# Kernel tuning notes

Measured on AMD Instinct MI355X. Metric: run time of the kernel, lower is better.

Reference implementation:

```python
import jax, jax.numpy as jnp
import numpy as np


def _expand_chunk(x):
    # prepend the previous bucket along the chunk axis: [b, nb, bl, ...] -> [b, nb, 2*bl, ...]
    return jnp.concatenate([jnp.roll(x, 1, axis=1), x], axis=2)


def _gather_seq(origin, idx):
    # origin [b, s, d], idx [b, s, r] -> out[b, s, :, r] = origin[b, idx[b, s, r], :]
    b = origin.shape[0]
    g = origin[jnp.arange(b)[:, None, None], idx]  # [b, s, r, d]
    return jnp.transpose(g, (0, 1, 3, 2))          # [b, s, d, r]


def _count_dup_keys(inp, rounds):
    # inp [b, s, K] int32: count duplicate key indices within a window of `rounds` in sorted order
    sort_idx = jnp.argsort(inp, axis=2)
    sorted_k = jnp.take_along_axis(inp, sort_idx, axis=2)
    unsort = jnp.argsort(sort_idx, axis=2)
    cnt = jnp.ones(inp.shape, jnp.float32)
    for i in range(1, rounds):
        eq = (sorted_k[..., i:] == sorted_k[..., :-i]).astype(jnp.float32)
        pad = jnp.zeros(inp.shape[:-1] + (i,), jnp.float32)
        cnt = cnt + jnp.concatenate([pad, eq], axis=-1) + jnp.concatenate([eq, pad], axis=-1)
    return jnp.take_along_axis(cnt, unsort, axis=2)


def setup_inputs() -> dict:
    key = jax.random.key(0)
    k1, k2, k3 = jax.random.split(key, 3)
    B_M_H, SEQ, D_K, N_ROUNDS, N_BUCKETS = 32, 2048, 64, 4, 32
    query = jax.random.normal(k1, (B_M_H, SEQ, D_K), jnp.float32)
    value = jax.random.normal(k2, (B_M_H, SEQ, D_K), jnp.float32)
    rand_matrix = jax.random.normal(k3, (B_M_H, D_K, N_ROUNDS, N_BUCKETS // 2), jnp.float32)
    return {"query": query, "value": value, "rand_matrix": rand_matrix}


def reference(query, value, rand_matrix):
    b, s, d = query.shape
    nr = rand_matrix.shape[2]
    n_buckets = 2 * rand_matrix.shape[3]
    bl = s // n_buckets  # bucket_len

    # --- LSH hashing: argmax over [proj, -proj], then make hashes unique per position ---
    proj = jnp.einsum('bsd,bdrk->bsrk', query, rand_matrix)
    hashes = jnp.argmax(jnp.concatenate([proj, -proj], axis=-1), axis=-1).astype(jnp.int32)
    hashes = hashes * s + jnp.arange(s, dtype=jnp.int32)[None, :, None]  # [b, s, nr]

    sort_idx = jnp.argsort(hashes, axis=1)      # [b, s, nr]
    unsort_idx = jnp.argsort(sort_idx, axis=1)  # [b, s, nr]

    # --- sort queries into buckets ---
    q = _gather_seq(query, sort_idx).reshape(b, n_buckets, bl, d, nr)
    k = _expand_chunk(q)  # [b, nb, 2*bl, d, nr]
    k = k * jax.lax.rsqrt(jnp.maximum(jnp.sum(k * k, axis=-2, keepdims=True), 1e-12))

    qk = jnp.einsum('bnidr,bnjdr->bnijr', q, k) / np.float32(np.sqrt(d))  # [b, nb, bl, 2bl, nr]

    # --- causal / self masks on original positions ---
    qi = sort_idx.reshape(b, n_buckets, bl, nr) % s
    ki = _expand_chunk(qi)  # [b, nb, 2bl, nr]
    mask1 = (qi[:, :, :, None, :] < ki[:, :, None, :, :]).astype(jnp.float32)
    mask2 = (qi[:, :, :, None, :] == ki[:, :, None, :, :]).astype(jnp.float32)
    qk = qk * (1 - mask1) + mask1 * (-1e9)
    qk = qk * (1 - mask2) + mask2 * (-1e5)

    # --- duplicate-key counting across rounds ---
    ki_b = jnp.broadcast_to(ki[:, :, None, :, :], (b, n_buckets, bl, 2 * bl, nr)).reshape(b, s, 2 * bl * nr)
    count_keys = _count_dup_keys(ki_b, nr).reshape(b, s, 2 * bl, nr)

    qk = qk.reshape(b, s, 2 * bl, nr)
    lse = jax.scipy.special.logsumexp(qk, axis=2)  # [b, s, nr]
    sm = jnp.exp(qk - lse[:, :, None, :]) / count_keys

    v = _gather_seq(value, sort_idx).reshape(b, n_buckets, bl, d, nr)
    vk = _expand_chunk(v)  # [b, nb, 2bl, d, nr]
    sm = sm.reshape(b, n_buckets, bl, 2 * bl, nr)
    att = jnp.einsum('bnijr,bnjdr->bnidr', sm, vk).reshape(b, s, d, nr)

    # --- unsort back to original order, per round ---
    att = jnp.transpose(att, (0, 1, 3, 2))  # [b, s, nr, d]
    att = jnp.take_along_axis(att, jnp.broadcast_to(unsort_idx[:, :, :, None], att.shape), axis=1)
    lse = jnp.take_along_axis(lse, unsort_idx, axis=1)

    # --- combine rounds weighted by softmax of logsumexp ---
    w = jax.nn.softmax(lse, axis=-1)  # [b, s, nr]
    return jnp.einsum('bsrd,bsr->bsd', att, w)
```

## Files before the change

### kernel.cpp

```cpp
#include <hip/hip_runtime.h>

typedef unsigned short u16;
typedef unsigned int   u32;
typedef short bf16x8 __attribute__((ext_vector_type(8)));
typedef float f32x16 __attribute__((ext_vector_type(16)));

#define S_  2048
#define D_  64
#define NR_ 4
#define NB_ 32

#define AS 72
#define VS 136
#define PS 136

__device__ __forceinline__ float bf2f(u16 u){ return __uint_as_float(((u32)u)<<16); }
__device__ __forceinline__ u16 f2bf(float f){
  u32 u = __float_as_uint(f);
  u32 r = (u + 0x7fffu + ((u>>16)&1u)) >> 16;
  return (u16)r;
}
__device__ __forceinline__ void unpack2(u32 w, float &a, float &b){
  a = __uint_as_float(w<<16);
  b = __uint_as_float(w & 0xffff0000u);
}
__device__ __forceinline__ bf16x8 ld8(const u16* p){
  union { uint4 u; bf16x8 v; } x;
  x.u = *(const uint4*)p;
  return x.v;
}

__global__ __launch_bounds__(256) void k_hash(const float* __restrict__ q,
                                              const float* __restrict__ R,
                                              int* __restrict__ hout){
  __shared__ float Rl[64][64];
  int b   = blockIdx.x >> 3;
  int pos = (blockIdx.x & 7) * 256 + threadIdx.x;
  const float* Rb = R + (size_t)b * 4096;
  for (int idx = threadIdx.x; idx < 4096; idx += 256)
    Rl[idx >> 6][idx & 63] = Rb[idx];
  __syncthreads();

  const float4* q4 = (const float4*)(q + ((size_t)b * S_ + pos) * D_);
  float acc[64];
  #pragma unroll
  for (int i = 0; i < 64; i++) acc[i] = 0.f;

  #pragma unroll
  for (int c = 0; c < 16; c++){
    float4 w = q4[c];
    float qd[4] = {w.x, w.y, w.z, w.w};
    #pragma unroll
    for (int dd = 0; dd < 4; dd++){
      int d = c * 4 + dd;
      const float4* Rr = (const float4*)(&Rl[d][0]);
      #pragma unroll
      for (int k4 = 0; k4 < 16; k4++){
        float4 rv = Rr[k4];
        acc[k4*4+0] += qd[dd] * rv.x;
        acc[k4*4+1] += qd[dd] * rv.y;
        acc[k4*4+2] += qd[dd] * rv.z;
        acc[k4*4+3] += qd[dd] * rv.w;
      }
    }
  }
  #pragma unroll
  for (int r = 0; r < 4; r++){
    float bv = acc[r*16]; int bi = 0;
    #pragma unroll
    for (int m = 1; m < 32; m++){
      float v = (m < 16) ? acc[r*16 + m] : -acc[r*16 + m - 16];
      if (v > bv){ bv = v; bi = m; }
    }
    hout[((size_t)b * NR_ + r) * S_ + pos] = bi;
  }
}

__global__ __launch_bounds__(256) void k_sort(const int* __restrict__ h,
                                              int* __restrict__ sidx,
                                              int* __restrict__ chk){
  __shared__ int cnt[32][257];
  __shared__ int base[32];
  int br = blockIdx.x;
  const int* hb = h + (size_t)br * S_;
  int t = threadIdx.x;

  #pragma unroll
  for (int hh = 0; hh < 32; hh++) cnt[hh][t] = 0;
  __syncthreads();

  int hv[8];
  const int4* hb4 = (const int4*)hb;
  int4 a0 = hb4[t*2], a1 = hb4[t*2+1];
  hv[0]=a0.x; hv[1]=a0.y; hv[2]=a0.z; hv[3]=a0.w;
  hv[4]=a1.x; hv[5]=a1.y; hv[6]=a1.z; hv[7]=a1.w;
  #pragma unroll
  for (int k = 0; k < 8; k++) cnt[hv[k]][t]++;
  __syncthreads();

  int wave = t >> 6, lane = t & 63;
  for (int hh = wave*8; hh < wave*8 + 8; hh++){
    int vals[4]; int s0 = 0;
    #pragma unroll
    for (int k = 0; k < 4; k++){ vals[k] = cnt[hh][lane*4+k]; s0 += vals[k]; }
    int incl = s0;
    #pragma unroll
    for (int off = 1; off < 64; off <<= 1){
      int o = __shfl_up(incl, off, 64);
      if (lane >= off) incl += o;
    }
    int run = incl - s0;
    #pragma unroll
    for (int k = 0; k < 4; k++){ int tmp = vals[k]; cnt[hh][lane*4+k] = run; run += tmp; }
    if (lane == 63) base[hh] = incl;
  }
  __syncthreads();
  if (t == 0){
    int run = 0;
    #pragma unroll
    for (int hh = 0; hh < 32; hh++){ int tot = base[hh]; base[hh] = run; run += tot; }
  }
  __syncthreads();

  int p0 = t * 8;
  #pragma unroll
  for (int k = 0; k < 8; k++){
    int hh = hv[k];
    int c = cnt[hh][t];
    int slot = base[hh] + c;
    cnt[hh][t] = c + 1;
    sidx[(size_t)br * S_ + slot]    = p0 + k;
    chk [(size_t)br * S_ + p0 + k]  = slot >> 6;
  }
}

__global__ __launch_bounds__(256, 4) void k_attn(const float* __restrict__ q,
                                                 const float* __restrict__ v,
                                                 const int* __restrict__ sidx,
                                                 const int* __restrict__ chk,
                                                 float* __restrict__ lse_ws,
                                                 u16*  __restrict__ att_ws){
  __shared__ u16 A[128*AS];
  __shared__ u16 SM[64*PS];
  __shared__ int   pkey[128];
  __shared__ float rcnt[128];
  __shared__ float sc[128];

  int blk = blockIdx.x;
  int b = blk >> 7, r = (blk >> 5) & 3, n = blk & 31;
  int npv = (n + 31) & 31;
  int t = threadIdx.x;
  int lane = t & 63, w = t >> 6;
  const int* sb = sidx + ((size_t)b * NR_ + r) * S_;

  if (t < 128){
    int p = (t < 64) ? sb[npv*64 + t] : sb[n*64 + (t - 64)];
    pkey[t] = p;
    int c = 0;
    #pragma unroll
    for (int rr = 0; rr < 4; rr++){
      int ch = chk[((size_t)b * NR_ + rr) * S_ + p];
      c += (ch == n) || (ch == npv);
    }
    if (c < 1) c = 1;
    rcnt[t] = 1.0f / (float)c;
  }
  __syncthreads();

  int row = t >> 1, half = t & 1;
  float4 qv[8];
  {
    const float4* src = (const float4*)(q + ((size_t)b*S_ + pkey[row])*D_) + half*8;
    #pragma unroll
    for (int k = 0; k < 8; k++) qv[k] = src[k];
  }
  int jp = t & 63, dgrp = t >> 6;
  float4 va[4], vb[4];
  {
    const float4* s0 = (const float4*)(v + ((size_t)b*S_ + pkey[2*jp  ])*D_) + dgrp*4;
    const float4* s1 = (const float4*)(v + ((size_t)b*S_ + pkey[2*jp+1])*D_) + dgrp*4;
    #pragma unroll
    for (int k = 0; k < 4; k++){ va[k] = s0[k]; vb[k] = s1[k]; }
  }
  {
    float ss = 0.f;
    u32 buf[16];
    #pragma unroll
    for (int k = 0; k < 8; k++){
      float4 f = qv[k];
      u16 b0 = f2bf(f.x), b1 = f2bf(f.y), b2 = f2bf(f.z), b3 = f2bf(f.w);
      float g0 = bf2f(b0), g1 = bf2f(b1), g2 = bf2f(b2), g3 = bf2f(b3);
      ss += g0*g0 + g1*g1 + g2*g2 + g3*g3;
      buf[k*2]   = (u32)b0 | ((u32)b1 << 16);
      buf[k*2+1] = (u32)b2 | ((u32)b3 << 16);
    }
    uint4* dst = (uint4*)(&A[row*AS + half*32]);
    #pragma unroll
    for (int k = 0; k < 4; k++)
      dst[k] = make_uint4(buf[4*k], buf[4*k+1], buf[4*k+2], buf[4*k+3]);
    float ss2 = ss + __shfl_xor(ss, 1, 64);
    if (half == 0) sc[row] = rsqrtf(fmaxf(ss2, 1e-12f)) * 0.125f;
  }
  __syncthreads();

  int Mt = w & 1, Nt0 = (w >> 1) * 2;
  f32x16 acc0, acc1;
  #pragma unroll
  for (int i = 0; i < 16; i++){ acc0[i] = 0.f; acc1[i] = 0.f; }
  {
    int mrow  = (64 + Mt*32 + (lane & 31)) * AS;
    int krow0 = (Nt0*32 + (lane & 31)) * AS;
    int krow1 = krow0 + 32*AS;
    int coff  = (lane >> 5) * 8;
    #pragma unroll
    for (int ks = 0; ks < 4; ks++){
      int o = ks*16 + coff;
      bf16x8 af = ld8(&A[mrow  + o]);
      bf16x8 b0 = ld8(&A[krow0 + o]);
      bf16x8 b1 = ld8(&A[krow1 + o]);
      acc0 = __builtin_amdgcn_mfma_f32_32x32x16_bf16(af, b0, acc0, 0, 0, 0);
      acc1 = __builtin_amdgcn_mfma_f32_32x32x16_bf16(af, b1, acc1, 0, 0, 0);
    }
  }
  {
    int h = lane >> 5;
    int pi[16];
    #pragma unroll
    for (int reg = 0; reg < 16; reg++){
      int il = (reg & 3) + 8*(reg >> 2) + 4*h;
      pi[reg] = pkey[64 + Mt*32 + il];
    }
    #pragma unroll
    for (int e = 0; e < 2; e++){
      int j = (Nt0 + e)*32 + (lane & 31);
      int pj = pkey[j];
      float scj = sc[j];
      #pragma unroll
      for (int reg = 0; reg < 16; reg++){
        int il = (reg & 3) + 8*(reg >> 2) + 4*h;
        float l = (e ? acc1[reg] : acc0[reg]) * scj;
        if (pi[reg] < pj)       l = -1000000000.0f;
        else if (pi[reg] == pj) l = -100000.0f;
        SM[(Mt*32 + il)*PS + j] = f2bf(l);
      }
    }
  }
  __syncthreads();

  {
    int srow = t >> 2, seg = t & 3;
    uint4 u[4];
    const uint4* p4 = (const uint4*)(&SM[srow*PS + seg*32]);
    #pragma unroll
    for (int k = 0; k < 4; k++) u[k] = p4[k];
    float vals[32];
    #pragma unroll
    for (int k = 0; k < 4; k++){
      unpack2(u[k].x, vals[k*8+0], vals[k*8+1]);
      unpack2(u[k].y, vals[k*8+2], vals[k*8+3]);
      unpack2(u[k].z, vals[k*8+4], vals[k*8+5]);
      unpack2(u[k].w, vals[k*8+6], vals[k*8+7]);
    }
    float mx = -3.0e38f;
    #pragma unroll
    for (int k = 0; k < 32; k++) mx = fmaxf(mx, vals[k]);
    mx = fmaxf(mx, __shfl_xor(mx, 1, 64));
    mx = fmaxf(mx, __shfl_xor(mx, 2, 64));
    float s = 0.f;
    #pragma unroll
    for (int k = 0; k < 32; k++) s += __expf(vals[k] - mx);
    s += __shfl_xor(s, 1, 64);
    s += __shfl_xor(s, 2, 64);
    float inv = 1.0f / s;
    u32 ob[16];
    #pragma unroll
    for (int k = 0; k < 16; k++){
      u16 p0 = f2bf(__expf(vals[2*k]   - mx) * inv);
      u16 p1 = f2bf(__expf(vals[2*k+1] - mx) * inv);
      ob[k] = (u32)p0 | ((u32)p1 << 16);
    }
    uint4* d4 = (uint4*)(&SM[srow*PS + seg*32]);
    #pragma unroll
    for (int k = 0; k < 4; k++)
      d4[k] = make_uint4(ob[4*k], ob[4*k+1], ob[4*k+2], ob[4*k+3]);
    if (seg == 0)
      lse_ws[((size_t)b*S_ + pkey[64 + srow])*NR_ + r] = mx + __logf(s);
  }
  __syncthreads();

  {
    float ra = rcnt[2*jp], rb = rcnt[2*jp+1];
    u32 vt[16];
    #pragma unroll
    for (int k = 0; k < 4; k++){
      float4 fa = va[k], fb = vb[k];
      vt[k*4+0] = (u32)f2bf(fa.x*ra) | ((u32)f2bf(fb.x*rb) << 16);
      vt[k*4+1] = (u32)f2bf(fa.y*ra) | ((u32)f2bf(fb.y*rb) << 16);
      vt[k*4+2] = (u32)f2bf(fa.z*ra) | ((u32)f2bf(fb.z*rb) << 16);
      vt[k*4+3] = (u32)f2bf(fa.w*ra) | ((u32)f2bf(fb.w*rb) << 16);
    }
    u32* vtp = (u32*)A;
    #pragma unroll
    for (int k = 0; k < 16; k++){
      int d = dgrp*16 + k;
      vtp[d*(VS/2) + jp] = vt[k];
    }
  }
  __syncthreads();

  {
    int Mt2 = w >> 1, Nt2 = w & 1;
    f32x16 acc;
    #pragma unroll
    for (int i = 0; i < 16; i++) acc[i] = 0.f;
    int prow = (Mt2*32 + (lane & 31)) * PS;
    int vrow = (Nt2*32 + (lane & 31)) * VS;
    int coff = (lane >> 5) * 8;
    #pragma unroll
    for (int ks = 0; ks < 8; ks++){
      int o = ks*16 + coff;
      bf16x8 af = ld8(&SM[prow + o]);
      bf16x8 bf = ld8(&A[vrow + o]);
      acc = __builtin_amdgcn_mfma_f32_32x32x16_bf16(af, bf, acc, 0, 0, 0);
    }
    int h = lane >> 5;
    int dcol = Nt2*32 + (lane & 31);
    #pragma unroll
    for (int reg = 0; reg < 16; reg++){
      int il = (reg & 3) + 8*(reg >> 2) + 4*h;
      int p = pkey[64 + Mt2*32 + il];
      att_ws[(((size_t)b*S_ + p)*NR_ + r)*D_ + dcol] = f2bf(acc[reg]);
    }
  }
}

__global__ __launch_bounds__(256) void k_comb(const float* __restrict__ lse_ws,
                                              const u16* __restrict__ att_ws,
                                              float* __restrict__ out){
  size_t idx = (size_t)blockIdx.x * 256 + threadIdx.x;
  size_t pd = idx >> 6;
  int d = (int)(idx & 63);
  float4 lv = *(const float4*)(lse_ws + pd * 4);
  float m = fmaxf(fmaxf(lv.x, lv.y), fmaxf(lv.z, lv.w));
  float e0 = __expf(lv.x - m), e1 = __expf(lv.y - m);
  float e2 = __expf(lv.z - m), e3 = __expf(lv.w - m);
  float inv = 1.0f / (e0 + e1 + e2 + e3);
  const u16* a = att_ws + pd * 256 + d;
  float o = (bf2f(a[0])   * e0 + bf2f(a[64])  * e1 +
             bf2f(a[128]) * e2 + bf2f(a[192]) * e3) * inv;
  out[idx] = o;
}

extern "C" void kernel_launch(void* const* d_in, const int* in_sizes, int n_in,
                              void* d_out, int out_size, void* d_ws, size_t ws_size,
                              hipStream_t stream){
  const float* q = (const float*)d_in[0];
  const float* v = (const float*)d_in[1];
  const float* R = (const float*)d_in[2];

  char* w = (char*)d_ws;
  int*   h    = (int*)  (w + 0);
  int*   sidx = (int*)  (w + (1u << 20));
  int*   chkA = (int*)  (w + (2u << 20));
  float* lse  = (float*)(w + (3u << 20));
  u16*   att  = (u16*)  (w + (4u << 20));
  float* out  = (float*)d_out;

  k_hash<<<256,  256, 0, stream>>>(q, R, h);
  k_sort<<<128,  256, 0, stream>>>(h, sidx, chkA);
  k_attn<<<4096, 256, 0, stream>>>(q, v, sidx, chkA, lse, att);
  k_comb<<<16384,256, 0, stream>>>(lse, att, out);
}
```

Baseline: 159.7 us.

## Precompute bf16 Q/V and row scales once; fold key counts into softmax

The hash kernel now also writes a bf16 copy of the queries and their per-row normalisation scale, and a new kernel converts values to bf16 once. The attention kernel, which otherwise reads each row four times (once per round), gathers half-size bf16 rows instead. The 1/count weighting moves from V into the softmax probabilities, which removes one barrier. The softmax reduction is reorganised to compute exponentials once, and bf16 packing uses a hardware convert builtin when available. In exchange there are extra launches and workspace traffic. The query norm is now taken from fp32 values rather than the rounded bf16 values, and the hash kernel reads R from global memory instead of LDS.

```diff
diff --git a/kernel.cpp b/kernel.cpp
--- a/kernel.cpp
+++ b/kernel.cpp
@@ -20,6 +20,15 @@
   u32 r = (u + 0x7fffu + ((u>>16)&1u)) >> 16;
   return (u16)r;
 }
+__device__ __forceinline__ u32 pk2bf(float a, float b){
+#if __has_builtin(__builtin_amdgcn_cvt_pk_bf16_f32)
+  auto r = __builtin_amdgcn_cvt_pk_bf16_f32(a, b);
+  u32 u; __builtin_memcpy(&u, &r, 4); return u;
+#else
+  return (u32)f2bf(a) | ((u32)f2bf(b) << 16);
+#endif
+}
+__device__ __forceinline__ u16 f2bf1(float a){ return (u16)pk2bf(a, a); }
 __device__ __forceinline__ void unpack2(u32 w, float &a, float &b){
   a = __uint_as_float(w<<16);
   b = __uint_as_float(w & 0xffff0000u);
@@ -32,31 +41,33 @@
 
 __global__ __launch_bounds__(256) void k_hash(const float* __restrict__ q,
                                               const float* __restrict__ R,
-                                              int* __restrict__ hout){
-  __shared__ float Rl[64][64];
+                                              int* __restrict__ hout,
+                                              u16* __restrict__ qb,
+                                              float* __restrict__ scq){
   int b   = blockIdx.x >> 3;
   int pos = (blockIdx.x & 7) * 256 + threadIdx.x;
-  const float* Rb = R + (size_t)b * 4096;
-  for (int idx = threadIdx.x; idx < 4096; idx += 256)
-    Rl[idx >> 6][idx & 63] = Rb[idx];
-  __syncthreads();
-
+  const float4* R4 = (const float4*)(R + (size_t)b * 4096);
   const float4* q4 = (const float4*)(q + ((size_t)b * S_ + pos) * D_);
+
   float acc[64];
   #pragma unroll
   for (int i = 0; i < 64; i++) acc[i] = 0.f;
+  u32 qp[32];
+  float ss = 0.f;
 
   #pragma unroll
   for (int c = 0; c < 16; c++){
     float4 w = q4[c];
+    ss += w.x*w.x + w.y*w.y + w.z*w.z + w.w*w.w;
+    qp[c*2]   = pk2bf(w.x, w.y);
+    qp[c*2+1] = pk2bf(w.z, w.w);
     float qd[4] = {w.x, w.y, w.z, w.w};
     #pragma unroll
     for (int dd = 0; dd < 4; dd++){
       int d = c * 4 + dd;
-      const float4* Rr = (const float4*)(&Rl[d][0]);
       #pragma unroll
       for (int k4 = 0; k4 < 16; k4++){
-        float4 rv = Rr[k4];
+        float4 rv = R4[d*16 + k4];
         acc[k4*4+0] += qd[dd] * rv.x;
         acc[k4*4+1] += qd[dd] * rv.y;
         acc[k4*4+2] += qd[dd] * rv.z;
@@ -64,6 +75,13 @@
       }
     }
   }
+  {
+    uint4* dst = (uint4*)(qb + ((size_t)b * S_ + pos) * D_);
+    #pragma unroll
+    for (int k = 0; k < 8; k++)
+      dst[k] = make_uint4(qp[4*k], qp[4*k+1], qp[4*k+2], qp[4*k+3]);
+    scq[(size_t)b * S_ + pos] = rsqrtf(fmaxf(ss, 1e-12f)) * 0.125f;
+  }
   #pragma unroll
   for (int r = 0; r < 4; r++){
     float bv = acc[r*16]; int bi = 0;
@@ -74,6 +92,13 @@
     }
     hout[((size_t)b * NR_ + r) * S_ + pos] = bi;
   }
+}
+
+__global__ __launch_bounds__(256) void k_prepv(const float* __restrict__ v,
+                                               u16* __restrict__ vb){
+  size_t idx = (size_t)blockIdx.x * 256 + threadIdx.x;
+  float4 f = ((const float4*)v)[idx];
+  ((uint2*)vb)[idx] = make_uint2(pk2bf(f.x, f.y), pk2bf(f.z, f.w));
 }
 
 __global__ __launch_bounds__(256) void k_sort(const int* __restrict__ h,
@@ -134,10 +159,11 @@
   }
 }
 
-__global__ __launch_bounds__(256, 4) void k_attn(const float* __restrict__ q,
-                                                 const float* __restrict__ v,
+__global__ __launch_bounds__(256, 4) void k_attn(const u16* __restrict__ qb,
+                                                 const u16* __restrict__ vb,
                                                  const int* __restrict__ sidx,
                                                  const int* __restrict__ chk,
+                                                 const float* __restrict__ scq,
                                                  float* __restrict__ lse_ws,
                                                  u16*  __restrict__ att_ws){
   __shared__ u16 A[128*AS];
@@ -164,42 +190,23 @@
     }
     if (c < 1) c = 1;
     rcnt[t] = 1.0f / (float)c;
-  }
-  __syncthreads();
-
-  int row = t >> 1, half = t & 1;
-  float4 qv[8];
-  {
-    const float4* src = (const float4*)(q + ((size_t)b*S_ + pkey[row])*D_) + half*8;
-    #pragma unroll
-    for (int k = 0; k < 8; k++) qv[k] = src[k];
+    sc[t] = scq[(size_t)b * S_ + p];
+  }
+  __syncthreads();
+
+  {
+    int row = t >> 1, half = t & 1;
+    const uint4* src = (const uint4*)(qb + ((size_t)b*S_ + pkey[row])*D_) + half*4;
+    uint4* dst = (uint4*)(&A[row*AS + half*32]);
+    #pragma unroll
+    for (int k = 0; k < 4; k++) dst[k] = src[k];
   }
   int jp = t & 63, dgrp = t >> 6;
-  float4 va[4], vb[4];
-  {
-    const float4* s0 = (const float4*)(v + ((size_t)b*S_ + pkey[2*jp  ])*D_) + dgrp*4;
-    const float4* s1 = (const float4*)(v + ((size_t)b*S_ + pkey[2*jp+1])*D_) + dgrp*4;
-    #pragma unroll
-    for (int k = 0; k < 4; k++){ va[k] = s0[k]; vb[k] = s1[k]; }
-  }
-  {
-    float ss = 0.f;
-    u32 buf[16];
-    #pragma unroll
-    for (int k = 0; k < 8; k++){
-      float4 f = qv[k];
-      u16 b0 = f2bf(f.x), b1 = f2bf(f.y), b2 = f2bf(f.z), b3 = f2bf(f.w);
-      float g0 = bf2f(b0), g1 = bf2f(b1), g2 = bf2f(b2), g3 = bf2f(b3);
-      ss += g0*g0 + g1*g1 + g2*g2 + g3*g3;
-      buf[k*2]   = (u32)b0 | ((u32)b1 << 16);
-      buf[k*2+1] = (u32)b2 | ((u32)b3 << 16);
-    }
-    uint4* dst = (uint4*)(&A[row*AS + half*32]);
-    #pragma unroll
-    for (int k = 0; k < 4; k++)
-      dst[k] = make_uint4(buf[4*k], buf[4*k+1], buf[4*k+2], buf[4*k+3]);
-    float ss2 = ss + __shfl_xor(ss, 1, 64);
-    if (half == 0) sc[row] = rsqrtf(fmaxf(ss2, 1e-12f)) * 0.125f;
+  uint4 va0, va1, vb0, vb1;
+  {
+    const uint4* s0 = (const uint4*)(vb + ((size_t)b*S_ + pkey[2*jp  ])*D_ + dgrp*16);
+    const uint4* s1 = (const uint4*)(vb + ((size_t)b*S_ + pkey[2*jp+1])*D_ + dgrp*16);
+    va0 = s0[0]; va1 = s0[1]; vb0 = s1[0]; vb1 = s1[1];
   }
   __syncthreads();
 
@@ -241,7 +248,7 @@
         float l = (e ? acc1[reg] : acc0[reg]) * scj;
         if (pi[reg] < pj)       l = -1000000000.0f;
         else if (pi[reg] == pj) l = -100000.0f;
-        SM[(Mt*32 + il)*PS + j] = f2bf(l);
+        SM[(Mt*32 + il)*PS + j] = f2bf1(l);
       }
     }
   }
@@ -264,46 +271,43 @@
     float mx = -3.0e38f;
     #pragma unroll
     for (int k = 0; k < 32; k++) mx = fmaxf(mx, vals[k]);
-    mx = fmaxf(mx, __shfl_xor(mx, 1, 64));
-    mx = fmaxf(mx, __shfl_xor(mx, 2, 64));
-    float s = 0.f;
-    #pragma unroll
-    for (int k = 0; k < 32; k++) s += __expf(vals[k] - mx);
+    float sl = 0.f;
+    #pragma unroll
+    for (int k = 0; k < 32; k++){ vals[k] = __expf(vals[k] - mx); sl += vals[k]; }
+    float mxg = fmaxf(mx, __shfl_xor(mx, 1, 64));
+    mxg = fmaxf(mxg, __shfl_xor(mxg, 2, 64));
+    float scale = __expf(mx - mxg);
+    float s = sl * scale;
     s += __shfl_xor(s, 1, 64);
     s += __shfl_xor(s, 2, 64);
-    float inv = 1.0f / s;
+    float f = scale / s;
+    const float4* rc4 = (const float4*)(&rcnt[seg*32]);
     u32 ob[16];
     #pragma unroll
-    for (int k = 0; k < 16; k++){
-      u16 p0 = f2bf(__expf(vals[2*k]   - mx) * inv);
-      u16 p1 = f2bf(__expf(vals[2*k+1] - mx) * inv);
-      ob[k] = (u32)p0 | ((u32)p1 << 16);
+    for (int k4 = 0; k4 < 8; k4++){
+      float4 rc = rc4[k4];
+      ob[k4*2+0] = pk2bf(vals[k4*4+0]*f*rc.x, vals[k4*4+1]*f*rc.y);
+      ob[k4*2+1] = pk2bf(vals[k4*4+2]*f*rc.z, vals[k4*4+3]*f*rc.w);
     }
     uint4* d4 = (uint4*)(&SM[srow*PS + seg*32]);
     #pragma unroll
     for (int k = 0; k < 4; k++)
       d4[k] = make_uint4(ob[4*k], ob[4*k+1], ob[4*k+2], ob[4*k+3]);
     if (seg == 0)
-      lse_ws[((size_t)b*S_ + pkey[64 + srow])*NR_ + r] = mx + __logf(s);
-  }
-  __syncthreads();
-
-  {
-    float ra = rcnt[2*jp], rb = rcnt[2*jp+1];
-    u32 vt[16];
-    #pragma unroll
-    for (int k = 0; k < 4; k++){
-      float4 fa = va[k], fb = vb[k];
-      vt[k*4+0] = (u32)f2bf(fa.x*ra) | ((u32)f2bf(fb.x*rb) << 16);
-      vt[k*4+1] = (u32)f2bf(fa.y*ra) | ((u32)f2bf(fb.y*rb) << 16);
-      vt[k*4+2] = (u32)f2bf(fa.z*ra) | ((u32)f2bf(fb.z*rb) << 16);
-      vt[k*4+3] = (u32)f2bf(fa.w*ra) | ((u32)f2bf(fb.w*rb) << 16);
-    }
+      lse_ws[((size_t)b*S_ + pkey[64 + srow])*NR_ + r] = mxg + __logf(s);
+  }
+
+  {
+    u32 au[8] = {va0.x, va0.y, va0.z, va0.w, va1.x, va1.y, va1.z, va1.w};
+    u32 bu[8] = {vb0.x, vb0.y, vb0.z, vb0.w, vb1.x, vb1.y, vb1.z, vb1.w};
     u32* vtp = (u32*)A;
     #pragma unroll
-    for (int k = 0; k < 16; k++){
-      int d = dgrp*16 + k;
-      vtp[d*(VS/2) + jp] = vt[k];
+    for (int k = 0; k < 8; k++){
+      int d0 = dgrp*16 + 2*k;
+      u32 even = (au[k] & 0xffffu) | (bu[k] << 16);
+      u32 odd  = (au[k] >> 16)     | (bu[k] & 0xffff0000u);
+      vtp[ d0      * (VS/2) + jp] = even;
+      vtp[(d0 + 1) * (VS/2) + jp] = odd;
     }
   }
   __syncthreads();
@@ -329,7 +333,7 @@
     for (int reg = 0; reg < 16; reg++){
       int il = (reg & 3) + 8*(reg >> 2) + 4*h;
       int p = pkey[64 + Mt2*32 + il];
-      att_ws[(((size_t)b*S_ + p)*NR_ + r)*D_ + dcol] = f2bf(acc[reg]);
+      att_ws[(((size_t)b*S_ + p)*NR_ + r)*D_ + dcol] = f2bf1(acc[reg]);
     }
   }
 }
@@ -360,14 +364,18 @@
 
   char* w = (char*)d_ws;
   int*   h    = (int*)  (w + 0);
-  int*   sidx = (int*)  (w + (1u << 20));
-  int*   chkA = (int*)  (w + (2u << 20));
-  float* lse  = (float*)(w + (3u << 20));
-  u16*   att  = (u16*)  (w + (4u << 20));
+  int*   sidx = (int*)  (w + (size_t)(1u << 20));
+  int*   chkA = (int*)  (w + (size_t)(2u << 20));
+  float* lse  = (float*)(w + (size_t)(3u << 20));
+  u16*   att  = (u16*)  (w + (size_t)(4u << 20));
+  u16*   qb   = (u16*)  (w + (size_t)(36u << 20));
+  u16*   vbuf = (u16*)  (w + (size_t)(44u << 20));
+  float* scq  = (float*)(w + (size_t)(52u << 20));
   float* out  = (float*)d_out;
 
-  k_hash<<<256,  256, 0, stream>>>(q, R, h);
-  k_sort<<<128,  256, 0, stream>>>(h, sidx, chkA);
-  k_attn<<<4096, 256, 0, stream>>>(q, v, sidx, chkA, lse, att);
-  k_comb<<<16384,256, 0, stream>>>(lse, att, out);
-}
+  k_hash <<<256,  256, 0, stream>>>(q, R, h, qb, scq);
+  k_prepv<<<4096, 256, 0, stream>>>(v, vbuf);
+  k_sort <<<128,  256, 0, stream>>>(h, sidx, chkA);
+  k_attn <<<4096, 256, 0, stream>>>(qb, vbuf, sidx, chkA, scq, lse, att);
+  k_comb <<<16384,256, 0, stream>>>(lse, att, out);
+}
```

Measured after the change: 212.0 us. 32.8% more time.
